# Kernel tuning notes

Hardware: AMD Instinct MI355X
Metric: run time of the kernel (lower is better)

Reference implementation:

```python
import math
import jax, jax.numpy as jnp
import numpy as np

N_HEAD = 16
KNN = 4                     # config.knn_num
MEM_FRAC = 8.0              # config.mem_frac
INFLUENCE = 1.0             # config.knn_softmax_influence
RESID_FOUND = 0.5           # from set_resid_frac(resid_frac=0.5) (assumed split)
RESID_CURR = 0.5


def setup_inputs() -> dict:
    key = jax.random.key(0)
    ks = jax.random.split(key, 7)
    B, T, C, H, M = 1, 1024, 1024, N_HEAD, 8192
    d = C // H
    return {
        "x": jax.random.normal(ks[0], (B, T, C), jnp.float32),
        "c_attn_w": jax.random.normal(ks[1], (3 * C, C), jnp.float32) * 0.02,
        "c_attn_b": jax.random.normal(ks[2], (3 * C,), jnp.float32) * 0.01,
        "c_proj_w": jax.random.normal(ks[3], (C, C), jnp.float32) * 0.02,
        "c_proj_b": jax.random.normal(ks[4], (C,), jnp.float32) * 0.01,
        "key_store": jax.random.normal(ks[5], (H, M, d), jnp.float32),
        "value_store": jax.random.normal(ks[6], (H, M, d), jnp.float32),
    }


def _knn_get(att, k, q, v, key_store, value_store):
    # Faithful vectorized version of knn_get (batch must be 1, as in the
    # original whose scatter offsets i*t are only valid for b==1).
    B, H, T, d = k.shape
    scale = 1.0 / math.sqrt(d)
    # last-query attention row over all keys: (B,H,T)
    a = att[:, :, -1, :]
    # mem_frac thresholding (bookkeeping_frac falsy -> skipped)
    a = jnp.where(a < 1.0 / (MEM_FRAC * T), 0.0, a)
    sel = (a != 0.0)[0]                      # (H,T) selected positions
    kh, qh, vh = k[0], q[0], v[0]            # (H,T,d)
    # exact L2 search = faiss.IndexFlatL2: d2 = |k|^2 - 2 k.s + |s|^2
    d2 = (jnp.sum(kh * kh, -1, keepdims=True)
          - 2.0 * jnp.einsum('htd,hmd->htm', kh, key_store)
          + jnp.sum(key_store * key_store, -1)[:, None, :])   # (H,T,M)
    _, idx = jax.lax.top_k(-d2, KNN)         # (H,T,K) nearest neighbors
    idx = jnp.maximum(idx, 0)                # idx[idx<0]=0
    keys_f = jnp.take_along_axis(key_store[:, None, :, :], idx[..., None], axis=2)   # (H,T,K,d)
    vals_f = jnp.take_along_axis(value_store[:, None, :, :], idx[..., None], axis=2)
    # not resid_only: prepend current key/value -> stack size K+1
    keys_all = jnp.concatenate([kh[:, :, None, :], keys_f], axis=2)   # (H,T,S,d)
    vals_all = jnp.concatenate([vh[:, :, None, :], vals_f], axis=2)
    attf = jnp.einsum('htd,htsd->hts', qh, keys_all) * scale
    attf = jnp.where(jnp.isnan(attf), -jnp.inf, attf)
    w = jax.nn.softmax(attf * INFLUENCE, axis=-1)                     # softmax over the stack dim
    vals = jnp.einsum('hts,htsd->htd', w, vals_all)
    vals = vals * RESID_FOUND + vh * RESID_CURR                       # resid mix branch
    v_new = jnp.where(sel[..., None], vals, vh)                       # scatter back
    return v_new[None]                                                # (1,H,T,d)


def reference(x, c_attn_w, c_attn_b, c_proj_w, c_proj_b, key_store, value_store):
    B, T, C = x.shape
    H = key_store.shape[0]
    d = C // H
    qkv = x @ c_attn_w.T + c_attn_b
    q, k, v = jnp.split(qkv, 3, axis=2)
    heads = lambda t: t.reshape(B, T, H, d).transpose(0, 2, 1, 3)
    q, k, v = heads(q), heads(k), heads(v)
    logits = jnp.einsum('bhqd,bhkd->bhqk', q, k) * (1.0 / math.sqrt(d))
    causal = jnp.tril(jnp.ones((T, T), bool))
    logits = jnp.where(causal, logits, -jnp.inf)
    att = jax.nn.softmax(logits, axis=-1)
    # knn_get runs under torch.no_grad in the original
    v_new = jax.lax.stop_gradient(_knn_get(att, k, q, v, key_store, value_store))
    y = jnp.einsum('bhqk,bhkd->bhqd', att, v_new)   # dropout p=0 (eval)
    y = y.transpose(0, 2, 1, 3).reshape(B, T, C)
    return y @ c_proj_w.T + c_proj_b
```

## Files before the change

kernel.cpp:

```cpp
#include <hip/hip_runtime.h>
#include <math.h>

#define NH 16
#define TT 1024
#define CC 1024
#define DD 64
#define MM 8192
#define MQ 4
#define MQS (MM / MQ)

typedef __attribute__((ext_vector_type(8))) short short8;
typedef __attribute__((ext_vector_type(4))) float f32x4;

__device__ __forceinline__ float wredsum(float x) {
#pragma unroll
  for (int o = 32; o; o >>= 1) x += __shfl_xor(x, o);
  return x;
}
__device__ __forceinline__ unsigned int bf16rn(float x) {
  unsigned int u = __float_as_uint(x);
  return (u + 0x7fffu + ((u >> 16) & 1u)) >> 16;
}
__device__ __forceinline__ float bf16f(unsigned int h) {
  return __uint_as_float(h << 16);
}

__device__ __forceinline__ void ins4(float d, int i, float vd[4], int vi[4]) {
  if (d < vd[3] || (d == vd[3] && i < vi[3])) {
    vd[3] = d; vi[3] = i;
#pragma unroll
    for (int s = 3; s > 0; --s) {
      bool sw = (vd[s] < vd[s - 1]) || (vd[s] == vd[s - 1] && vi[s] < vi[s - 1]);
      if (sw) {
        float td = vd[s]; vd[s] = vd[s - 1]; vd[s - 1] = td;
        int ti = vi[s]; vi[s] = vi[s - 1]; vi[s - 1] = ti;
      }
    }
  }
}

__device__ __forceinline__ void stage_rows8_swz(const char* gRow0, size_t gStride, char* lds, int lane) {
  int rr = lane >> 3;
  int c = (lane & 7) ^ rr;
  __builtin_amdgcn_global_load_lds(
      (const __attribute__((address_space(1))) unsigned int*)(gRow0 + (size_t)rr * gStride + (c << 4)),
      (__attribute__((address_space(3))) unsigned int*)lds, 16, 0, 0);
}

__device__ __forceinline__ void conv_chunk(const float* __restrict__ src,
                                           char* __restrict__ hi, char* __restrict__ lo, int gc) {
  const float* p = src + ((size_t)gc << 3);
  float4 f0 = *(const float4*)p;
  float4 f1 = *(const float4*)(p + 4);
  float f[8] = {f0.x, f0.y, f0.z, f0.w, f1.x, f1.y, f1.z, f1.w};
  short8 hv, lv;
#pragma unroll
  for (int e = 0; e < 8; ++e) {
    unsigned hb = bf16rn(f[e]);
    hv[e] = (short)hb;
    lv[e] = (short)bf16rn(f[e] - bf16f(hb));
  }
  size_t off = (size_t)gc << 4;
  *(short8*)(hi + off) = hv;
  *(short8*)(lo + off) = lv;
}

__device__ __forceinline__ void conv_chunk_hi(const float* __restrict__ src,
                                              char* __restrict__ hi, int gc) {
  const float* p = src + ((size_t)gc << 3);
  float4 f0 = *(const float4*)p;
  float4 f1 = *(const float4*)(p + 4);
  float f[8] = {f0.x, f0.y, f0.z, f0.w, f1.x, f1.y, f1.z, f1.w};
  short8 hv;
#pragma unroll
  for (int e = 0; e < 8; ++e) hv[e] = (short)bf16rn(f[e]);
  *(short8*)(hi + ((size_t)gc << 4)) = hv;
}

__global__ void __launch_bounds__(256) convert_all(
    const float* __restrict__ x, char* __restrict__ xhi, char* __restrict__ xlo,
    const float* __restrict__ Wa, char* __restrict__ wahi, char* __restrict__ walo,
    const float* __restrict__ Wp, char* __restrict__ wphi,
    const float* __restrict__ ks, char* __restrict__ khi, char* __restrict__ klo,
    float* __restrict__ kn2)
{
  int b = blockIdx.x, tid = threadIdx.x;
  if (b < 512) { conv_chunk(x, xhi, xlo, b * 256 + tid); return; }
  if (b < 2048) {
    int gc = (b - 512) * 256 + tid;
    if (gc < 262144) conv_chunk(Wa, wahi, walo, gc);
    else conv_chunk_hi(Wa, wahi, gc);
    return;
  }
  if (b < 2560) { conv_chunk_hi(Wp, wphi, (b - 2048) * 256 + tid); return; }
  int gc = (b - 2560) * 256 + tid;
  const float* p = ks + ((size_t)gc << 3);
  float4 f0 = *(const float4*)p;
  float4 f1 = *(const float4*)(p + 4);
  float f[8] = {f0.x, f0.y, f0.z, f0.w, f1.x, f1.y, f1.z, f1.w};
  float s = 0.f;
  short8 hv, lv;
#pragma unroll
  for (int e = 0; e < 8; ++e) {
    s = fmaf(f[e], f[e], s);
    unsigned hb = bf16rn(f[e]);
    hv[e] = (short)hb;
    lv[e] = (short)bf16rn(f[e] - bf16f(hb));
  }
  size_t off = (size_t)gc << 4;
  *(short8*)(khi + off) = hv;
  *(short8*)(klo + off) = lv;
  s += __shfl_xor(s, 1);
  s += __shfl_xor(s, 2);
  s += __shfl_xor(s, 4);
  if ((tid & 7) == 0) kn2[gc >> 3] = -0.5f * s;
}

__global__ void __launch_bounds__(256) gemm_qkv(
    const char* __restrict__ xhi, const char* __restrict__ xlo,
    const char* __restrict__ wahi, const char* __restrict__ walo,
    const float* __restrict__ ba, char* __restrict__ qhi, char* __restrict__ qlo)
{
  int n0 = blockIdx.x * 128, m0 = blockIdx.y * 64;
  bool vsec = (n0 >= 2048);
  int tid = threadIdx.x, lane = tid & 63, w = tid >> 6;
  int wr = w >> 1, wc = w & 1;
  int lr = lane & 15, lc = lane >> 4;
  __shared__ __align__(16) char smem[49152];
  char* sAhi = smem;
  char* sAlo = smem + 8192;
  char* sBhi = smem + 16384;
  char* sBlo = smem + 32768;
  f32x4 acc[2][4];
#pragma unroll
  for (int i = 0; i < 2; ++i)
#pragma unroll
    for (int j = 0; j < 4; ++j) acc[i][j] = (f32x4){0.f, 0.f, 0.f, 0.f};

  for (int kb = 0; kb < 16; ++kb) {
    if (kb) __syncthreads();
#pragma unroll
    for (int c8 = 0; c8 < 2; ++c8) {
      int r8 = w * 16 + c8 * 8;
      stage_rows8_swz(xhi + (size_t)(m0 + r8) * 2048 + (size_t)kb * 128, 2048, sAhi + r8 * 128, lane);
      if (!vsec)
        stage_rows8_swz(xlo + (size_t)(m0 + r8) * 2048 + (size_t)kb * 128, 2048, sAlo + r8 * 128, lane);
    }
#pragma unroll
    for (int c8 = 0; c8 < 4; ++c8) {
      int r8 = w * 32 + c8 * 8;
      stage_rows8_swz(wahi + (size_t)(n0 + r8) * 2048 + (size_t)kb * 128, 2048, sBhi + r8 * 128, lane);
      if (!vsec)
        stage_rows8_swz(walo + (size_t)(n0 + r8) * 2048 + (size_t)kb * 128, 2048, sBlo + r8 * 128, lane);
    }
    __syncthreads();
#pragma unroll
    for (int kh = 0; kh < 2; ++kh) {
      short8 ah[2], al[2], bh[4], bl[4];
#pragma unroll
      for (int mi = 0; mi < 2; ++mi) {
        int ra = wr * 32 + mi * 16 + lr;
        int ca = ((kh * 4 + lc) ^ (ra & 7)) << 4;
        ah[mi] = *(const short8*)(sAhi + ra * 128 + ca);
        if (!vsec) al[mi] = *(const short8*)(sAlo + ra * 128 + ca);
      }
#pragma unroll
      for (int nj = 0; nj < 4; ++nj) {
        int rb = wc * 64 + nj * 16 + lr;
        int cb = ((kh * 4 + lc) ^ (rb & 7)) << 4;
        bh[nj] = *(const short8*)(sBhi + rb * 128 + cb);
        if (!vsec) bl[nj] = *(const short8*)(sBlo + rb * 128 + cb);
      }
      if (!vsec) {
#pragma unroll
        for (int mi = 0; mi < 2; ++mi)
#pragma unroll
          for (int nj = 0; nj < 4; ++nj) {
            acc[mi][nj] = __builtin_amdgcn_mfma_f32_16x16x32_bf16(ah[mi], bh[nj], acc[mi][nj], 0, 0, 0);
            acc[mi][nj] = __builtin_amdgcn_mfma_f32_16x16x32_bf16(al[mi], bh[nj], acc[mi][nj], 0, 0, 0);
            acc[mi][nj] = __builtin_amdgcn_mfma_f32_16x16x32_bf16(ah[mi], bl[nj], acc[mi][nj], 0, 0, 0);
          }
      } else {
#pragma unroll
        for (int mi = 0; mi < 2; ++mi)
#pragma unroll
          for (int nj = 0; nj < 4; ++nj)
            acc[mi][nj] = __builtin_amdgcn_mfma_f32_16x16x32_bf16(ah[mi], bh[nj], acc[mi][nj], 0, 0, 0);
      }
    }
  }

  __syncthreads();
  char* hbuf = smem + w * 9216;
  char* lbuf = hbuf + 4608;
#pragma unroll
  for (int mi = 0; mi < 2; ++mi)
#pragma unroll
    for (int nj = 0; nj < 4; ++nj)
#pragma unroll
      for (int r = 0; r < 4; ++r) {
        int row = mi * 16 + lc * 4 + r;
        int col = nj * 16 + lr;
        float v = acc[mi][nj][r] + ba[n0 + wc * 64 + col];
        unsigned hb = bf16rn(v);
        *(unsigned short*)(hbuf + row * 144 + col * 2) = (unsigned short)hb;
        if (!vsec)
          *(unsigned short*)(lbuf + row * 144 + col * 2) = (unsigned short)bf16rn(v - bf16f(hb));
      }
#pragma unroll
  for (int ps = 0; ps < 4; ++ps) {
    int rr = ps * 8 + (lane >> 3);
    int c = lane & 7;
    size_t gb = ((size_t)(m0 + wr * 32 + rr) * 3072 + n0 + wc * 64) * 2 + (c << 4);
    *(uint4*)(qhi + gb) = *(const uint4*)(hbuf + rr * 144 + c * 16);
    if (!vsec) *(uint4*)(qlo + gb) = *(const uint4*)(lbuf + rr * 144 + c * 16);
  }
}

#define QSLDS 2304
__global__ void __launch_bounds__(512) qk_softmax(
    const char* __restrict__ qhi, const char* __restrict__ qlo,
    char* __restrict__ attB, float* __restrict__ attlast)
{
  int rb = blockIdx.x, h = blockIdx.y;
  int i0 = rb * 32;
  bool full = (rb == 31);
  int tid = threadIdx.x, lane = tid & 63, w = tid >> 6;
  int wr = w >> 2, wcg = w & 3;
  int lr = lane & 15, lc = lane >> 4;
  __shared__ float redm[2][16][4];
  __shared__ float reds[2][16][4];
  __shared__ __align__(16) char tb[8][QSLDS];

  int iq = i0 + wr * 16 + lr;
  short8 ah[2];
  short8 al[2] = {short8{0,0,0,0,0,0,0,0}, short8{0,0,0,0,0,0,0,0}};
  {
    size_t qb = (size_t)iq * 6144 + h * 128;
#pragma unroll
    for (int kh = 0; kh < 2; ++kh)
      ah[kh] = *(const short8*)(qhi + qb + ((kh * 4 + lc) << 4));
    if (full) {
#pragma unroll
      for (int kh = 0; kh < 2; ++kh)
        al[kh] = *(const short8*)(qlo + qb + ((kh * 4 + lc) << 4));
    }
  }

  f32x4 acc[16];
#pragma unroll
  for (int nt = 0; nt < 16; ++nt) acc[nt] = (f32x4){0.f, 0.f, 0.f, 0.f};

  int maxj = i0 + 31;
#pragma unroll
  for (int nt = 0; nt < 16; ++nt) {
    if (wcg * 256 + nt * 16 <= maxj) {
      int jr = wcg * 256 + nt * 16 + lr;
      size_t kb = (size_t)jr * 6144 + 2048 + h * 128;
      short8 bh[2];
#pragma unroll
      for (int kh = 0; kh < 2; ++kh)
        bh[kh] = *(const short8*)(qhi + kb + ((kh * 4 + lc) << 4));
      if (full) {
        short8 bl[2];
#pragma unroll
        for (int kh = 0; kh < 2; ++kh)
          bl[kh] = *(const short8*)(qlo + kb + ((kh * 4 + lc) << 4));
#pragma unroll
        for (int kh = 0; kh < 2; ++kh) {
          acc[nt] = __builtin_amdgcn_mfma_f32_16x16x32_bf16(ah[kh], bh[kh], acc[nt], 0, 0, 0);
          acc[nt] = __builtin_amdgcn_mfma_f32_16x16x32_bf16(al[kh], bh[kh], acc[nt], 0, 0, 0);
          acc[nt] = __builtin_amdgcn_mfma_f32_16x16x32_bf16(ah[kh], bl[kh], acc[nt], 0, 0, 0);
        }
      } else {
#pragma unroll
        for (int kh = 0; kh < 2; ++kh)
          acc[nt] = __builtin_amdgcn_mfma_f32_16x16x32_bf16(ah[kh], bh[kh], acc[nt], 0, 0, 0);
      }
    }
  }

  int iv[4];
  float pmax[4];
#pragma unroll
  for (int r = 0; r < 4; ++r) {
    iv[r] = i0 + wr * 16 + lc * 4 + r;
    pmax[r] = -INFINITY;
  }
#pragma unroll
  for (int nt = 0; nt < 16; ++nt) {
    if (wcg * 256 + nt * 16 <= maxj) {
      int j = wcg * 256 + nt * 16 + lr;
#pragma unroll
      for (int r = 0; r < 4; ++r) {
        float v = (j <= iv[r]) ? acc[nt][r] * 0.125f : -INFINITY;
        acc[nt][r] = v;
        pmax[r] = fmaxf(pmax[r], v);
      }
    }
  }
#pragma unroll
  for (int o = 1; o <= 8; o <<= 1)
#pragma unroll
    for (int r = 0; r < 4; ++r) pmax[r] = fmaxf(pmax[r], __shfl_xor(pmax[r], o));
  if (lr == 0) {
#pragma unroll
    for (int r = 0; r < 4; ++r) redm[wr][lc * 4 + r][wcg] = pmax[r];
  }
  __syncthreads();
  float rowm[4];
#pragma unroll
  for (int r = 0; r < 4; ++r) {
    float* q = redm[wr][lc * 4 + r];
    rowm[r] = fmaxf(fmaxf(q[0], q[1]), fmaxf(q[2], q[3]));
  }

  float psum[4] = {0.f, 0.f, 0.f, 0.f};
#pragma unroll
  for (int nt = 0; nt < 16; ++nt) {
    if (wcg * 256 + nt * 16 <= maxj) {
#pragma unroll
      for (int r = 0; r < 4; ++r) {
        float e = __expf(acc[nt][r] - rowm[r]);
        acc[nt][r] = e;
        psum[r] += e;
      }
    }
  }
#pragma unroll
  for (int o = 1; o <= 8; o <<= 1)
#pragma unroll
    for (int r = 0; r < 4; ++r) psum[r] += __shfl_xor(psum[r], o);
  if (lr == 0) {
#pragma unroll
    for (int r = 0; r < 4; ++r) reds[wr][lc * 4 + r][wcg] = psum[r];
  }
  __syncthreads();
  float inv[4];
#pragma unroll
  for (int r = 0; r < 4; ++r) {
    float* q = reds[wr][lc * 4 + r];
    inv[r] = 1.0f / (q[0] + q[1] + q[2] + q[3]);
  }

  char* mybuf = tb[w];
  int iv0 = i0 + wr * 16;
  int limit128 = (i0 & ~127) + 128;
#pragma unroll
  for (int cc = 0; cc < 4; ++cc) {
    if (wcg * 256 + cc * 64 < limit128) {
#pragma unroll
      for (int q = 0; q < 4; ++q) {
        int nt = cc * 4 + q;
        int col = q * 16 + lr;
#pragma unroll
        for (int r = 0; r < 4; ++r) {
          int row = lc * 4 + r;
          float v = acc[nt][r] * inv[r];
          *(unsigned short*)(mybuf + row * 144 + col * 2) = (unsigned short)bf16rn(v);
          if (iv[r] == 1023) attlast[(h << 10) + wcg * 256 + cc * 64 + col] = v;
        }
      }
#pragma unroll
      for (int half = 0; half < 2; ++half) {
        int rr = (lane >> 3) + half * 8;
        int c = lane & 7;
        int rowg = iv0 + rr;
        uint4 hv = *(const uint4*)(mybuf + rr * 144 + c * 16);
        size_t basep = ((size_t)h << 21) + ((size_t)rowg << 11)
                     + (size_t)(((wcg << 2) + cc) << 7) + (size_t)(c << 4);
        *(uint4*)(attB + basep) = hv;
      }
    }
  }
}

#define BUFB 16384

#define TOPK_STEP(PAR, DO_STAGE)                                              \
  {                                                                           \
    if (DO_STAGE) {                                                           \
      _Pragma("unroll")                                                       \
      for (int i2 = 0; i2 < 4; ++i2) {                                        \
        __builtin_amdgcn_global_load_lds(                                     \
            (const __attribute__((address_space(1))) unsigned int*)stsrc[i2], \
            (__attribute__((address_space(3))) unsigned int*)(stdst[i2] + ((PAR) ^ 16384)), \
            16, 0, 0);                                                        \
        stsrc[i2] += 8192;                                                    \
      }                                                                       \
    }                                                                         \
    f32x4 acc[4];                                                             \
    _Pragma("unroll")                                                         \
    for (int ms = 0; ms < 4; ++ms)                                            \
      acc[ms] = *(const f32x4*)(knp + ms * 64);                               \
    knp += 256;                                                               \
    _Pragma("unroll")                                                         \
    for (int ms = 0; ms < 4; ++ms) {                                          \
      short8 ah0 = *(const short8*)(frg[ms * 2 + 0] + (PAR));                 \
      short8 al0 = *(const short8*)(frg[ms * 2 + 0] + (PAR) + 8192);          \
      short8 ah1 = *(const short8*)(frg[ms * 2 + 1] + (PAR));                 \
      short8 al1 = *(const short8*)(frg[ms * 2 + 1] + (PAR) + 8192);          \
      acc[ms] = __builtin_amdgcn_mfma_f32_16x16x32_bf16(ah0, bhi[0], acc[ms], 0, 0, 0); \
      acc[ms] = __builtin_amdgcn_mfma_f32_16x16x32_bf16(al0, bhi[0], acc[ms], 0, 0, 0); \
      acc[ms] = __builtin_amdgcn_mfma_f32_16x16x32_bf16(ah0, blo[0], acc[ms], 0, 0, 0); \
      acc[ms] = __builtin_amdgcn_mfma_f32_16x16x32_bf16(ah1, bhi[1], acc[ms], 0, 0, 0); \
      acc[ms] = __builtin_amdgcn_mfma_f32_16x16x32_bf16(al1, bhi[1], acc[ms], 0, 0, 0); \
      acc[ms] = __builtin_amdgcn_mfma_f32_16x16x32_bf16(ah1, blo[1], acc[ms], 0, 0, 0); \
    }                                                                         \
    float pk[16];                                                             \
    _Pragma("unroll")                                                         \
    for (int ms = 0; ms < 4; ++ms)                                            \
      _Pragma("unroll")                                                       \
      for (int r = 0; r < 4; ++r) {                                           \
        unsigned u = __float_as_uint(acc[ms][r]);                             \
        pk[ms * 4 + r] = __uint_as_float((u & ~15u) | (unsigned)(ms * 4 + r)); \
      }                                                                       \
    float mx = pk[0];                                                         \
    _Pragma("unroll")                                                         \
    for (int c = 1; c < 16; ++c) mx = fmaxf(mx, pk[c]);                       \
    while (mx > ba[3]) {                                                      \
      unsigned pb = __float_as_uint(mx);                                      \
      int cl = pb & 15;                                                       \
      ba[3] = mx; bi_[3] = mg0 + ((cl & 12) << 2) + (cl & 3);                 \
      _Pragma("unroll")                                                       \
      for (int s = 3; s > 0; --s)                                             \
        if (ba[s] > ba[s - 1]) {                                              \
          float td = ba[s]; ba[s] = ba[s - 1]; ba[s - 1] = td;                \
          int ti = bi_[s]; bi_[s] = bi_[s - 1]; bi_[s - 1] = ti;              \
        }                                                                     \
      _Pragma("unroll")                                                       \
      for (int c2 = 0; c2 < 16; ++c2)                                         \
        if (pk[c2] == mx) pk[c2] = -3.0e38f;                                  \
      mx = pk[0];                                                             \
      _Pragma("unroll")                                                       \
      for (int c2 = 1; c2 < 16; ++c2) mx = fmaxf(mx, pk[c2]);                 \
    }                                                                         \
    mg0 += 64;                                                                \
    __syncthreads();                                                          \
  }

__global__ void __launch_bounds__(256, 4) topk_mfma(
    const char* __restrict__ qhi, const char* __restrict__ qlo,
    const char* __restrict__ khi, const char* __restrict__ klo,
    const float* __restrict__ kn2, float* __restrict__ pd, int* __restrict__ pi)
{
  int bid = blockIdx.x;
  int h = bid & 15, ttile = (bid >> 4) & 15, mq = bid >> 8;
  int tid = threadIdx.x, lane = tid & 63, w = tid >> 6;
  int t0 = ttile * 64 + w * 16;
  __shared__ __align__(16) char smem[2 * BUFB];

  short8 bhi[2], blo[2];
  {
    int t = t0 + (lane & 15);
    size_t rb = (size_t)t * 6144 + 2048 + h * 128;
#pragma unroll
    for (int kh = 0; kh < 2; ++kh) {
      size_t off = rb + ((kh * 4 + (lane >> 4)) << 4);
      bhi[kh] = *(const short8*)(qhi + off);
      blo[kh] = *(const short8*)(qlo + off);
    }
  }

  const char* ghi = khi + ((size_t)h * MM + (size_t)mq * MQS) * 128;
  const char* glo = klo + ((size_t)h * MM + (size_t)mq * MQS) * 128;
  const char* knp = (const char*)(kn2 + (size_t)h * MM + (size_t)mq * MQS + ((lane >> 4) << 2));

  float ba[4] = {-3.0e38f, -3.0e38f, -3.0e38f, -3.0e38f};
  int   bi_[4] = {-1, -1, -1, -1};

  const char* stsrc[4];
  char* stdst[4];
  {
    int rr = lane >> 3;
    size_t laneoff = (size_t)rr * 128 + (((lane & 7) ^ rr) << 4);
#pragma unroll
    for (int i2 = 0; i2 < 4; ++i2) {
      int s = w * 4 + i2;
      stsrc[i2] = ((s < 8) ? (ghi + s * 1024) : (glo + (s - 8) * 1024)) + laneoff;
      stdst[i2] = smem + s * 1024;
    }
  }
  char* frg[8];
#pragma unroll
  for (int ms = 0; ms < 4; ++ms)
#pragma unroll
    for (int kh = 0; kh < 2; ++kh) {
      int mloc = ms * 16 + (lane & 15);
      int c = kh * 4 + (lane >> 4);
      frg[ms * 2 + kh] = smem + mloc * 128 + ((c ^ (mloc & 7)) << 4);
    }

#pragma unroll
  for (int i2 = 0; i2 < 4; ++i2) {
    __builtin_amdgcn_global_load_lds(
        (const __attribute__((address_space(1))) unsigned int*)stsrc[i2],
        (__attribute__((address_space(3))) unsigned int*)stdst[i2], 16, 0, 0);
    stsrc[i2] += 8192;
  }
  __syncthreads();

  int mg0 = mq * MQS + ((lane >> 4) << 2);
  for (int it2 = 0; it2 < 16; ++it2) {
    TOPK_STEP(0, true)
    TOPK_STEP(16384, (it2 < 15))
  }

  float bd[4];
#pragma unroll
  for (int s = 0; s < 4; ++s) bd[s] = ba[s] * -2.0f;
#pragma unroll
  for (int st = 16; st <= 32; st <<= 1) {
    float sd[4]; int si[4];
#pragma unroll
    for (int s = 0; s < 4; ++s) {
      sd[s] = __shfl_xor(bd[s], st);
      si[s] = __shfl_xor(bi_[s], st);
    }
#pragma unroll
    for (int s = 0; s < 4; ++s) ins4(sd[s], si[s], bd, bi_);
  }
  if (lane < 16) {
    size_t o = (((size_t)mq * NH + h) * TT + (t0 + lane)) * 4;
#pragma unroll
    for (int s = 0; s < 4; ++s) { pd[o + s] = bd[s]; pi[o + s] = bi_[s]; }
  }
}

__global__ void __launch_bounds__(1024) knn_attend(
    const char* __restrict__ qhi,
    const float* __restrict__ attlast,
    const float* __restrict__ pd, const int* __restrict__ pi,
    const float* __restrict__ kstore, const float* __restrict__ vstore,
    char* __restrict__ vThi)
{
  __shared__ __align__(16) unsigned short hiT[64][72];
  int tid = threadIdx.x, lane = tid & 63, w = tid >> 6;
  int h = blockIdx.x >> 4, t0 = (blockIdx.x & 15) << 6;

#pragma unroll
  for (int i = 0; i < 4; ++i) {
    int t = t0 + w * 4 + i;
    int g = (h << 10) + t;

    float fd[4]; int fi[4];
    {
      size_t o = ((size_t)(lane & 3) * (NH * TT) + g) * 4;
#pragma unroll
      for (int s = 0; s < 4; ++s) { fd[s] = pd[o + s]; fi[s] = pi[o + s]; }
#pragma unroll
      for (int st = 1; st <= 2; st <<= 1) {
        float sd[4]; int si[4];
#pragma unroll
        for (int s = 0; s < 4; ++s) {
          sd[s] = __shfl_xor(fd[s], st);
          si[s] = __shfl_xor(fi[s], st);
        }
#pragma unroll
        for (int s = 0; s < 4; ++s) ins4(sd[s], si[s], fd, fi);
      }
    }

    size_t rbq = (size_t)t * 6144 + h * 128 + lane * 2;
    float q = bf16f(*(const unsigned short*)(qhi + rbq));
    float k = bf16f(*(const unsigned short*)(qhi + rbq + 2048));
    float v = bf16f(*(const unsigned short*)(qhi + rbq + 4096));
    float al = attlast[g];
    bool sel = al >= (1.0f / 8192.0f);

    float attf[5], vf[5];
    attf[0] = wredsum(q * k) * 0.125f;
    vf[0] = v;
#pragma unroll
    for (int s = 1; s < 5; ++s) {
      int m = fi[s - 1];
      const float* kp = kstore + ((size_t)h * MM + m) * DD;
      const float* vp = vstore + ((size_t)h * MM + m) * DD;
      attf[s] = wredsum(q * kp[lane]) * 0.125f;
      vf[s] = vp[lane];
    }
    float mx = attf[0];
#pragma unroll
    for (int s = 1; s < 5; ++s) mx = fmaxf(mx, attf[s]);
    float wgt[5], sum = 0.f;
#pragma unroll
    for (int s = 0; s < 5; ++s) { wgt[s] = __expf(attf[s] - mx); sum += wgt[s]; }
    float inv = 1.0f / sum;
    float vals = 0.f;
#pragma unroll
    for (int s = 0; s < 5; ++s) vals = fmaf(wgt[s] * inv, vf[s], vals);
    float r = 0.5f * vals + 0.5f * v;
    float vn = sel ? r : v;

    hiT[lane][t - t0] = (unsigned short)bf16rn(vn);
  }
  __syncthreads();

  if (tid < 512) {
    int r = tid >> 3, c = tid & 7;
    uint4 vv = *(const uint4*)&hiT[r][c * 8];
    char* dst = vThi + (size_t)((h << 6) + r) * 2048 + ((size_t)t0 << 1) + (c << 4);
    *(uint4*)dst = vv;
  }
}

__global__ void __launch_bounds__(256) gemm_attv(
    const char* __restrict__ attB, const char* __restrict__ vThi,
    char* __restrict__ Yhi)
{
  int h = blockIdx.y, m0 = blockIdx.x * 64;
  const char* aBase = attB + ((size_t)h << 21);
  int tid = threadIdx.x, lane = tid & 63, w = tid >> 6;
  int wr = w >> 1, wc = w & 1;
  __shared__ __align__(16) char smem[16384];
  char* sAhi = smem;
  char* sBhi = smem + 8192;
  f32x4 acc[2][2];
#pragma unroll
  for (int i = 0; i < 2; ++i)
#pragma unroll
    for (int j = 0; j < 2; ++j) acc[i][j] = (f32x4){0.f, 0.f, 0.f, 0.f};
  int lr = lane & 15, lc = lane >> 4;
  int kbEnd = (m0 >> 6) + 1;
  for (int kb = 0; kb < kbEnd; ++kb) {
    if (kb) __syncthreads();
#pragma unroll
    for (int c8 = 0; c8 < 2; ++c8) {
      int r8 = w * 16 + c8 * 8;
      stage_rows8_swz(aBase + (size_t)(m0 + r8) * 2048 + (size_t)kb * 128, 2048, sAhi + r8 * 128, lane);
      stage_rows8_swz(vThi + (size_t)((h << 6) + r8) * 2048 + (size_t)kb * 128, 2048, sBhi + r8 * 128, lane);
    }
    __syncthreads();
#pragma unroll
    for (int kh = 0; kh < 2; ++kh) {
      short8 ah[2], bh[2];
#pragma unroll
      for (int f = 0; f < 2; ++f) {
        int ra = wr * 32 + f * 16 + lr;
        int ca = ((kh * 4 + lc) ^ (ra & 7)) << 4;
        ah[f] = *(const short8*)(sAhi + ra * 128 + ca);
        int rbr = wc * 32 + f * 16 + lr;
        int cb = ((kh * 4 + lc) ^ (rbr & 7)) << 4;
        bh[f] = *(const short8*)(sBhi + rbr * 128 + cb);
      }
#pragma unroll
      for (int mi = 0; mi < 2; ++mi)
#pragma unroll
        for (int nj = 0; nj < 2; ++nj)
          acc[mi][nj] = __builtin_amdgcn_mfma_f32_16x16x32_bf16(ah[mi], bh[nj], acc[mi][nj], 0, 0, 0);
    }
  }
#pragma unroll
  for (int mi = 0; mi < 2; ++mi)
#pragma unroll
    for (int nj = 0; nj < 2; ++nj)
#pragma unroll
      for (int r = 0; r < 4; ++r) {
        int m = m0 + wr * 32 + mi * 16 + lc * 4 + r;
        int n = (h << 6) + wc * 32 + nj * 16 + lr;
        size_t off = ((size_t)m * 1024 + n) * 2;
        *(unsigned short*)(Yhi + off) = (unsigned short)bf16rn(acc[mi][nj][r]);
      }
}

__global__ void __launch_bounds__(256) gemm_out(
    const char* __restrict__ yhi,
    const char* __restrict__ wphi,
    const float* __restrict__ bp, float* __restrict__ out)
{
  int n0 = blockIdx.x * 64, m0 = blockIdx.y * 64;
  int tid = threadIdx.x, lane = tid & 63, w = tid >> 6;
  int wr = w >> 1, wc = w & 1;
  int lr = lane & 15, lc = lane >> 4;
  __shared__ __align__(16) char smem[16384];
  char* sAhi = smem;
  char* sBhi = smem + 8192;
  f32x4 acc[2][2];
#pragma unroll
  for (int i = 0; i < 2; ++i)
#pragma unroll
    for (int j = 0; j < 2; ++j) acc[i][j] = (f32x4){0.f, 0.f, 0.f, 0.f};

  for (int kb = 0; kb < 16; ++kb) {
    if (kb) __syncthreads();
#pragma unroll
    for (int c8 = 0; c8 < 2; ++c8) {
      int r8 = w * 16 + c8 * 8;
      stage_rows8_swz(yhi + (size_t)(m0 + r8) * 2048 + (size_t)kb * 128, 2048, sAhi + r8 * 128, lane);
      stage_rows8_swz(wphi + (size_t)(n0 + r8) * 2048 + (size_t)kb * 128, 2048, sBhi + r8 * 128, lane);
    }
    __syncthreads();
#pragma unroll
    for (int kh = 0; kh < 2; ++kh) {
      short8 ah[2], bh[2];
#pragma unroll
      for (int mi = 0; mi < 2; ++mi) {
        int ra = wr * 32 + mi * 16 + lr;
        int ca = ((kh * 4 + lc) ^ (ra & 7)) << 4;
        ah[mi] = *(const short8*)(sAhi + ra * 128 + ca);
      }
#pragma unroll
      for (int nj = 0; nj < 2; ++nj) {
        int rb = wc * 32 + nj * 16 + lr;
        int cb = ((kh * 4 + lc) ^ (rb & 7)) << 4;
        bh[nj] = *(const short8*)(sBhi + rb * 128 + cb);
      }
#pragma unroll
      for (int mi = 0; mi < 2; ++mi)
#pragma unroll
        for (int nj = 0; nj < 2; ++nj)
          acc[mi][nj] = __builtin_amdgcn_mfma_f32_16x16x32_bf16(ah[mi], bh[nj], acc[mi][nj], 0, 0, 0);
    }
  }
#pragma unroll
  for (int mi = 0; mi < 2; ++mi)
#pragma unroll
    for (int nj = 0; nj < 2; ++nj)
#pragma unroll
      for (int r = 0; r < 4; ++r) {
        int m = m0 + wr * 32 + mi * 16 + lc * 4 + r;
        int n = n0 + wc * 32 + nj * 16 + lr;
        out[(size_t)m * 1024 + n] = acc[mi][nj][r] + bp[n];
      }
}

extern "C" void kernel_launch(void* const* d_in, const int* in_sizes, int n_in,
                              void* d_out, int out_size, void* d_ws, size_t ws_size,
                              hipStream_t stream) {
  (void)in_sizes; (void)n_in; (void)out_size; (void)ws_size;
  const float* x  = (const float*)d_in[0];
  const float* Wa = (const float*)d_in[1];
  const float* ba = (const float*)d_in[2];
  const float* Wp = (const float*)d_in[3];
  const float* bp = (const float*)d_in[4];
  const float* Ks = (const float*)d_in[5];
  const float* Vs = (const float*)d_in[6];
  float* out = (float*)d_out;

  char* base = (char*)d_ws;
  char* xhi  = base;
  char* xlo  = base + 0x200000;
  char* wahi = base + 0x400000;
  char* walo = base + 0xA00000;
  char* khi  = base + 0x1000000;
  char* klo  = base + 0x2000000;
  char*  attB = base;
  char* tail = base + 0x4000000;
  char* qhi = tail;
  char* qlo = tail + 0x600000;
  float* attlast = (float*)(tail + 0xC00000);
  float* kn2     = (float*)(tail + 0xC10000);
  float* pd      = (float*)(tail + 0xC90000);
  int*   pi      = (int*)(tail + 0xE90000);
  char* vThi = tail + 0x1090000;
  char* yhi  = tail + 0x1290000;
  char* wphi = tail + 0x1490000;

  hipLaunchKernelGGL(convert_all, dim3(6656), dim3(256), 0, stream,
                     x, xhi, xlo, Wa, wahi, walo, Wp, wphi, Ks, khi, klo, kn2);
  hipLaunchKernelGGL(gemm_qkv, dim3(24, 16), dim3(256), 0, stream,
                     (const char*)xhi, (const char*)xlo, (const char*)wahi, (const char*)walo,
                     ba, qhi, qlo);
  hipLaunchKernelGGL(topk_mfma, dim3(16 * 16 * MQ), dim3(256), 0, stream,
                     (const char*)qhi, (const char*)qlo, (const char*)khi, (const char*)klo,
                     kn2, pd, pi);
  hipLaunchKernelGGL(qk_softmax, dim3(32, 16), dim3(512), 0, stream,
                     (const char*)qhi, (const char*)qlo, attB, attlast);
  hipLaunchKernelGGL(knn_attend, dim3(256), dim3(1024), 0, stream,
                     (const char*)qhi, attlast, pd, pi, Ks, Vs, vThi);
  hipLaunchKernelGGL(gemm_attv, dim3(16, 16), dim3(256), 0, stream,
                     (const char*)attB, (const char*)vThi, yhi);
  hipLaunchKernelGGL(gemm_out, dim3(16, 16), dim3(256), 0, stream,
                     (const char*)yhi, (const char*)wphi, bp, out);
}
```

Measured before the change: 195.3 us.

## Fuse top-k search and QK softmax into one heterogeneous launch

Merges the independent topk_mfma and qk_softmax kernels into a single 1024-block launch. Even blocks run two top-k units side by side (256 threads each, each with its own 32KB LDS half), and odd blocks run one softmax row-block. The aim is to overlap the memory-bound top-k scan with the softmax work and drop one launch. The key store buffers are moved so they no longer alias attB, which is now written concurrently. In exchange, every block reserves 64KB of shared memory and uses 512 threads, which may lower occupancy for the top-k work.

```diff
diff --git a/kernel.cpp b/kernel.cpp
--- a/kernel.cpp
+++ b/kernel.cpp
@@ -217,165 +217,8 @@
   }
 }
 
+#define BUFB 16384
 #define QSLDS 2304
-__global__ void __launch_bounds__(512) qk_softmax(
-    const char* __restrict__ qhi, const char* __restrict__ qlo,
-    char* __restrict__ attB, float* __restrict__ attlast)
-{
-  int rb = blockIdx.x, h = blockIdx.y;
-  int i0 = rb * 32;
-  bool full = (rb == 31);
-  int tid = threadIdx.x, lane = tid & 63, w = tid >> 6;
-  int wr = w >> 2, wcg = w & 3;
-  int lr = lane & 15, lc = lane >> 4;
-  __shared__ float redm[2][16][4];
-  __shared__ float reds[2][16][4];
-  __shared__ __align__(16) char tb[8][QSLDS];
-
-  int iq = i0 + wr * 16 + lr;
-  short8 ah[2];
-  short8 al[2] = {short8{0,0,0,0,0,0,0,0}, short8{0,0,0,0,0,0,0,0}};
-  {
-    size_t qb = (size_t)iq * 6144 + h * 128;
-#pragma unroll
-    for (int kh = 0; kh < 2; ++kh)
-      ah[kh] = *(const short8*)(qhi + qb + ((kh * 4 + lc) << 4));
-    if (full) {
-#pragma unroll
-      for (int kh = 0; kh < 2; ++kh)
-        al[kh] = *(const short8*)(qlo + qb + ((kh * 4 + lc) << 4));
-    }
-  }
-
-  f32x4 acc[16];
-#pragma unroll
-  for (int nt = 0; nt < 16; ++nt) acc[nt] = (f32x4){0.f, 0.f, 0.f, 0.f};
-
-  int maxj = i0 + 31;
-#pragma unroll
-  for (int nt = 0; nt < 16; ++nt) {
-    if (wcg * 256 + nt * 16 <= maxj) {
-      int jr = wcg * 256 + nt * 16 + lr;
-      size_t kb = (size_t)jr * 6144 + 2048 + h * 128;
-      short8 bh[2];
-#pragma unroll
-      for (int kh = 0; kh < 2; ++kh)
-        bh[kh] = *(const short8*)(qhi + kb + ((kh * 4 + lc) << 4));
-      if (full) {
-        short8 bl[2];
-#pragma unroll
-        for (int kh = 0; kh < 2; ++kh)
-          bl[kh] = *(const short8*)(qlo + kb + ((kh * 4 + lc) << 4));
-#pragma unroll
-        for (int kh = 0; kh < 2; ++kh) {
-          acc[nt] = __builtin_amdgcn_mfma_f32_16x16x32_bf16(ah[kh], bh[kh], acc[nt], 0, 0, 0);
-          acc[nt] = __builtin_amdgcn_mfma_f32_16x16x32_bf16(al[kh], bh[kh], acc[nt], 0, 0, 0);
-          acc[nt] = __builtin_amdgcn_mfma_f32_16x16x32_bf16(ah[kh], bl[kh], acc[nt], 0, 0, 0);
-        }
-      } else {
-#pragma unroll
-        for (int kh = 0; kh < 2; ++kh)
-          acc[nt] = __builtin_amdgcn_mfma_f32_16x16x32_bf16(ah[kh], bh[kh], acc[nt], 0, 0, 0);
-      }
-    }
-  }
-
-  int iv[4];
-  float pmax[4];
-#pragma unroll
-  for (int r = 0; r < 4; ++r) {
-    iv[r] = i0 + wr * 16 + lc * 4 + r;
-    pmax[r] = -INFINITY;
-  }
-#pragma unroll
-  for (int nt = 0; nt < 16; ++nt) {
-    if (wcg * 256 + nt * 16 <= maxj) {
-      int j = wcg * 256 + nt * 16 + lr;
-#pragma unroll
-      for (int r = 0; r < 4; ++r) {
-        float v = (j <= iv[r]) ? acc[nt][r] * 0.125f : -INFINITY;
-        acc[nt][r] = v;
-        pmax[r] = fmaxf(pmax[r], v);
-      }
-    }
-  }
-#pragma unroll
-  for (int o = 1; o <= 8; o <<= 1)
-#pragma unroll
-    for (int r = 0; r < 4; ++r) pmax[r] = fmaxf(pmax[r], __shfl_xor(pmax[r], o));
-  if (lr == 0) {
-#pragma unroll
-    for (int r = 0; r < 4; ++r) redm[wr][lc * 4 + r][wcg] = pmax[r];
-  }
-  __syncthreads();
-  float rowm[4];
-#pragma unroll
-  for (int r = 0; r < 4; ++r) {
-    float* q = redm[wr][lc * 4 + r];
-    rowm[r] = fmaxf(fmaxf(q[0], q[1]), fmaxf(q[2], q[3]));
-  }
-
-  float psum[4] = {0.f, 0.f, 0.f, 0.f};
-#pragma unroll
-  for (int nt = 0; nt < 16; ++nt) {
-    if (wcg * 256 + nt * 16 <= maxj) {
-#pragma unroll
-      for (int r = 0; r < 4; ++r) {
-        float e = __expf(acc[nt][r] - rowm[r]);
-        acc[nt][r] = e;
-        psum[r] += e;
-      }
-    }
-  }
-#pragma unroll
-  for (int o = 1; o <= 8; o <<= 1)
-#pragma unroll
-    for (int r = 0; r < 4; ++r) psum[r] += __shfl_xor(psum[r], o);
-  if (lr == 0) {
-#pragma unroll
-    for (int r = 0; r < 4; ++r) reds[wr][lc * 4 + r][wcg] = psum[r];
-  }
-  __syncthreads();
-  float inv[4];
-#pragma unroll
-  for (int r = 0; r < 4; ++r) {
-    float* q = reds[wr][lc * 4 + r];
-    inv[r] = 1.0f / (q[0] + q[1] + q[2] + q[3]);
-  }
-
-  char* mybuf = tb[w];
-  int iv0 = i0 + wr * 16;
-  int limit128 = (i0 & ~127) + 128;
-#pragma unroll
-  for (int cc = 0; cc < 4; ++cc) {
-    if (wcg * 256 + cc * 64 < limit128) {
-#pragma unroll
-      for (int q = 0; q < 4; ++q) {
-        int nt = cc * 4 + q;
-        int col = q * 16 + lr;
-#pragma unroll
-        for (int r = 0; r < 4; ++r) {
-          int row = lc * 4 + r;
-          float v = acc[nt][r] * inv[r];
-          *(unsigned short*)(mybuf + row * 144 + col * 2) = (unsigned short)bf16rn(v);
-          if (iv[r] == 1023) attlast[(h << 10) + wcg * 256 + cc * 64 + col] = v;
-        }
-      }
-#pragma unroll
-      for (int half = 0; half < 2; ++half) {
-        int rr = (lane >> 3) + half * 8;
-        int c = lane & 7;
-        int rowg = iv0 + rr;
-        uint4 hv = *(const uint4*)(mybuf + rr * 144 + c * 16);
-        size_t basep = ((size_t)h << 21) + ((size_t)rowg << 11)
-                     + (size_t)(((wcg << 2) + cc) << 7) + (size_t)(c << 4);
-        *(uint4*)(attB + basep) = hv;
-      }
-    }
-  }
-}
-
-#define BUFB 16384
 
 #define TOPK_STEP(PAR, DO_STAGE)                                              \
   {                                                                           \
@@ -439,91 +282,252 @@
     __syncthreads();                                                          \
   }
 
-__global__ void __launch_bounds__(256, 4) topk_mfma(
+__global__ void __launch_bounds__(512, 4) fused_topk_qk(
     const char* __restrict__ qhi, const char* __restrict__ qlo,
     const char* __restrict__ khi, const char* __restrict__ klo,
-    const float* __restrict__ kn2, float* __restrict__ pd, int* __restrict__ pi)
+    const float* __restrict__ kn2, float* __restrict__ pd, int* __restrict__ pi,
+    char* __restrict__ attB, float* __restrict__ attlast)
 {
+  __shared__ __align__(16) char smem[65536];
   int bid = blockIdx.x;
-  int h = bid & 15, ttile = (bid >> 4) & 15, mq = bid >> 8;
-  int tid = threadIdx.x, lane = tid & 63, w = tid >> 6;
-  int t0 = ttile * 64 + w * 16;
-  __shared__ __align__(16) char smem[2 * BUFB];
-
-  short8 bhi[2], blo[2];
-  {
-    int t = t0 + (lane & 15);
-    size_t rb = (size_t)t * 6144 + 2048 + h * 128;
-#pragma unroll
-    for (int kh = 0; kh < 2; ++kh) {
-      size_t off = rb + ((kh * 4 + (lane >> 4)) << 4);
-      bhi[kh] = *(const short8*)(qhi + off);
-      blo[kh] = *(const short8*)(qlo + off);
-    }
-  }
-
-  const char* ghi = khi + ((size_t)h * MM + (size_t)mq * MQS) * 128;
-  const char* glo = klo + ((size_t)h * MM + (size_t)mq * MQS) * 128;
-  const char* knp = (const char*)(kn2 + (size_t)h * MM + (size_t)mq * MQS + ((lane >> 4) << 2));
-
-  float ba[4] = {-3.0e38f, -3.0e38f, -3.0e38f, -3.0e38f};
-  int   bi_[4] = {-1, -1, -1, -1};
-
-  const char* stsrc[4];
-  char* stdst[4];
-  {
-    int rr = lane >> 3;
-    size_t laneoff = (size_t)rr * 128 + (((lane & 7) ^ rr) << 4);
+  int tid = threadIdx.x;
+
+  if ((bid & 1) == 0) {
+    int uid = (bid & ~1) + (tid >> 8);
+    char* usmem = smem + ((tid >> 8) << 15);
+    int ltid = tid & 255;
+    int h = uid & 15, ttile = (uid >> 4) & 15, mq = uid >> 8;
+    int lane = ltid & 63, w = ltid >> 6;
+    int t0 = ttile * 64 + w * 16;
+
+    short8 bhi[2], blo[2];
+    {
+      int t = t0 + (lane & 15);
+      size_t rb = (size_t)t * 6144 + 2048 + h * 128;
+#pragma unroll
+      for (int kh = 0; kh < 2; ++kh) {
+        size_t off = rb + ((kh * 4 + (lane >> 4)) << 4);
+        bhi[kh] = *(const short8*)(qhi + off);
+        blo[kh] = *(const short8*)(qlo + off);
+      }
+    }
+
+    const char* ghi = khi + ((size_t)h * MM + (size_t)mq * MQS) * 128;
+    const char* glo = klo + ((size_t)h * MM + (size_t)mq * MQS) * 128;
+    const char* knp = (const char*)(kn2 + (size_t)h * MM + (size_t)mq * MQS + ((lane >> 4) << 2));
+
+    float ba[4] = {-3.0e38f, -3.0e38f, -3.0e38f, -3.0e38f};
+    int   bi_[4] = {-1, -1, -1, -1};
+
+    const char* stsrc[4];
+    char* stdst[4];
+    {
+      int rr = lane >> 3;
+      size_t laneoff = (size_t)rr * 128 + (((lane & 7) ^ rr) << 4);
+#pragma unroll
+      for (int i2 = 0; i2 < 4; ++i2) {
+        int s = w * 4 + i2;
+        stsrc[i2] = ((s < 8) ? (ghi + s * 1024) : (glo + (s - 8) * 1024)) + laneoff;
+        stdst[i2] = usmem + s * 1024;
+      }
+    }
+    char* frg[8];
+#pragma unroll
+    for (int ms = 0; ms < 4; ++ms)
+#pragma unroll
+      for (int kh = 0; kh < 2; ++kh) {
+        int mloc = ms * 16 + (lane & 15);
+        int c = kh * 4 + (lane >> 4);
+        frg[ms * 2 + kh] = usmem + mloc * 128 + ((c ^ (mloc & 7)) << 4);
+      }
+
 #pragma unroll
     for (int i2 = 0; i2 < 4; ++i2) {
-      int s = w * 4 + i2;
-      stsrc[i2] = ((s < 8) ? (ghi + s * 1024) : (glo + (s - 8) * 1024)) + laneoff;
-      stdst[i2] = smem + s * 1024;
-    }
-  }
-  char* frg[8];
-#pragma unroll
-  for (int ms = 0; ms < 4; ++ms)
-#pragma unroll
-    for (int kh = 0; kh < 2; ++kh) {
-      int mloc = ms * 16 + (lane & 15);
-      int c = kh * 4 + (lane >> 4);
-      frg[ms * 2 + kh] = smem + mloc * 128 + ((c ^ (mloc & 7)) << 4);
-    }
-
-#pragma unroll
-  for (int i2 = 0; i2 < 4; ++i2) {
-    __builtin_amdgcn_global_load_lds(
-        (const __attribute__((address_space(1))) unsigned int*)stsrc[i2],
-        (__attribute__((address_space(3))) unsigned int*)stdst[i2], 16, 0, 0);
-    stsrc[i2] += 8192;
-  }
-  __syncthreads();
-
-  int mg0 = mq * MQS + ((lane >> 4) << 2);
-  for (int it2 = 0; it2 < 16; ++it2) {
-    TOPK_STEP(0, true)
-    TOPK_STEP(16384, (it2 < 15))
-  }
-
-  float bd[4];
-#pragma unroll
-  for (int s = 0; s < 4; ++s) bd[s] = ba[s] * -2.0f;
-#pragma unroll
-  for (int st = 16; st <= 32; st <<= 1) {
-    float sd[4]; int si[4];
-#pragma unroll
-    for (int s = 0; s < 4; ++s) {
-      sd[s] = __shfl_xor(bd[s], st);
-      si[s] = __shfl_xor(bi_[s], st);
-    }
-#pragma unroll
-    for (int s = 0; s < 4; ++s) ins4(sd[s], si[s], bd, bi_);
-  }
-  if (lane < 16) {
-    size_t o = (((size_t)mq * NH + h) * TT + (t0 + lane)) * 4;
-#pragma unroll
-    for (int s = 0; s < 4; ++s) { pd[o + s] = bd[s]; pi[o + s] = bi_[s]; }
+      __builtin_amdgcn_global_load_lds(
+          (const __attribute__((address_space(1))) unsigned int*)stsrc[i2],
+          (__attribute__((address_space(3))) unsigned int*)stdst[i2], 16, 0, 0);
+      stsrc[i2] += 8192;
+    }
+    __syncthreads();
+
+    int mg0 = mq * MQS + ((lane >> 4) << 2);
+    for (int it2 = 0; it2 < 16; ++it2) {
+      TOPK_STEP(0, true)
+      TOPK_STEP(16384, (it2 < 15))
+    }
+
+    float bd[4];
+#pragma unroll
+    for (int s = 0; s < 4; ++s) bd[s] = ba[s] * -2.0f;
+#pragma unroll
+    for (int st = 16; st <= 32; st <<= 1) {
+      float sd[4]; int si[4];
+#pragma unroll
+      for (int s = 0; s < 4; ++s) {
+        sd[s] = __shfl_xor(bd[s], st);
+        si[s] = __shfl_xor(bi_[s], st);
+      }
+#pragma unroll
+      for (int s = 0; s < 4; ++s) ins4(sd[s], si[s], bd, bi_);
+    }
+    if (lane < 16) {
+      size_t o = (((size_t)mq * NH + h) * TT + (t0 + lane)) * 4;
+#pragma unroll
+      for (int s = 0; s < 4; ++s) { pd[o + s] = bd[s]; pi[o + s] = bi_[s]; }
+    }
+  } else {
+    int qb = bid >> 1;
+    int rb = qb & 31, h = qb >> 5;
+    int i0 = rb * 32;
+    bool full = (rb == 31);
+    int lane = tid & 63, w = tid >> 6;
+    int wr = w >> 2, wcg = w & 3;
+    int lr = lane & 15, lc = lane >> 4;
+    float (*redm)[16][4] = (float (*)[16][4])smem;
+    float (*reds)[16][4] = (float (*)[16][4])(smem + 512);
+    char* tbb = smem + 1024;
+
+    int iq = i0 + wr * 16 + lr;
+    short8 ah[2];
+    short8 al[2] = {short8{0,0,0,0,0,0,0,0}, short8{0,0,0,0,0,0,0,0}};
+    {
+      size_t qb2 = (size_t)iq * 6144 + h * 128;
+#pragma unroll
+      for (int kh = 0; kh < 2; ++kh)
+        ah[kh] = *(const short8*)(qhi + qb2 + ((kh * 4 + lc) << 4));
+      if (full) {
+#pragma unroll
+        for (int kh = 0; kh < 2; ++kh)
+          al[kh] = *(const short8*)(qlo + qb2 + ((kh * 4 + lc) << 4));
+      }
+    }
+
+    f32x4 acc[16];
+#pragma unroll
+    for (int nt = 0; nt < 16; ++nt) acc[nt] = (f32x4){0.f, 0.f, 0.f, 0.f};
+
+    int maxj = i0 + 31;
+#pragma unroll
+    for (int nt = 0; nt < 16; ++nt) {
+      if (wcg * 256 + nt * 16 <= maxj) {
+        int jr = wcg * 256 + nt * 16 + lr;
+        size_t kb = (size_t)jr * 6144 + 2048 + h * 128;
+        short8 bh[2];
+#pragma unroll
+        for (int kh = 0; kh < 2; ++kh)
+          bh[kh] = *(const short8*)(qhi + kb + ((kh * 4 + lc) << 4));
+        if (full) {
+          short8 bl[2];
+#pragma unroll
+          for (int kh = 0; kh < 2; ++kh)
+            bl[kh] = *(const short8*)(qlo + kb + ((kh * 4 + lc) << 4));
+#pragma unroll
+          for (int kh = 0; kh < 2; ++kh) {
+            acc[nt] = __builtin_amdgcn_mfma_f32_16x16x32_bf16(ah[kh], bh[kh], acc[nt], 0, 0, 0);
+            acc[nt] = __builtin_amdgcn_mfma_f32_16x16x32_bf16(al[kh], bh[kh], acc[nt], 0, 0, 0);
+            acc[nt] = __builtin_amdgcn_mfma_f32_16x16x32_bf16(ah[kh], bl[kh], acc[nt], 0, 0, 0);
+          }
+        } else {
+#pragma unroll
+          for (int kh = 0; kh < 2; ++kh)
+            acc[nt] = __builtin_amdgcn_mfma_f32_16x16x32_bf16(ah[kh], bh[kh], acc[nt], 0, 0, 0);
+        }
+      }
+    }
+
+    int iv[4];
+    float pmax[4];
+#pragma unroll
+    for (int r = 0; r < 4; ++r) {
+      iv[r] = i0 + wr * 16 + lc * 4 + r;
+      pmax[r] = -INFINITY;
+    }
+#pragma unroll
+    for (int nt = 0; nt < 16; ++nt) {
+      if (wcg * 256 + nt * 16 <= maxj) {
+        int j = wcg * 256 + nt * 16 + lr;
+#pragma unroll
+        for (int r = 0; r < 4; ++r) {
+          float v = (j <= iv[r]) ? acc[nt][r] * 0.125f : -INFINITY;
+          acc[nt][r] = v;
+          pmax[r] = fmaxf(pmax[r], v);
+        }
+      }
+    }
+#pragma unroll
+    for (int o = 1; o <= 8; o <<= 1)
+#pragma unroll
+      for (int r = 0; r < 4; ++r) pmax[r] = fmaxf(pmax[r], __shfl_xor(pmax[r], o));
+    if (lr == 0) {
+#pragma unroll
+      for (int r = 0; r < 4; ++r) redm[wr][lc * 4 + r][wcg] = pmax[r];
+    }
+    __syncthreads();
+    float rowm[4];
+#pragma unroll
+    for (int r = 0; r < 4; ++r) {
+      float* q = redm[wr][lc * 4 + r];
+      rowm[r] = fmaxf(fmaxf(q[0], q[1]), fmaxf(q[2], q[3]));
+    }
+
+    float psum[4] = {0.f, 0.f, 0.f, 0.f};
+#pragma unroll
+    for (int nt = 0; nt < 16; ++nt) {
+      if (wcg * 256 + nt * 16 <= maxj) {
+#pragma unroll
+        for (int r = 0; r < 4; ++r) {
+          float e = __expf(acc[nt][r] - rowm[r]);
+          acc[nt][r] = e;
+          psum[r] += e;
+        }
+      }
+    }
+#pragma unroll
+    for (int o = 1; o <= 8; o <<= 1)
+#pragma unroll
+      for (int r = 0; r < 4; ++r) psum[r] += __shfl_xor(psum[r], o);
+    if (lr == 0) {
+#pragma unroll
+      for (int r = 0; r < 4; ++r) reds[wr][lc * 4 + r][wcg] = psum[r];
+    }
+    __syncthreads();
+    float inv[4];
+#pragma unroll
+    for (int r = 0; r < 4; ++r) {
+      float* q = reds[wr][lc * 4 + r];
+      inv[r] = 1.0f / (q[0] + q[1] + q[2] + q[3]);
+    }
+
+    char* mybuf = tbb + w * QSLDS;
+    int iv0 = i0 + wr * 16;
+    int limit128 = (i0 & ~127) + 128;
+#pragma unroll
+    for (int cc = 0; cc < 4; ++cc) {
+      if (wcg * 256 + cc * 64 < limit128) {
+#pragma unroll
+        for (int q = 0; q < 4; ++q) {
+          int nt = cc * 4 + q;
+          int col = q * 16 + lr;
+#pragma unroll
+          for (int r = 0; r < 4; ++r) {
+            int row = lc * 4 + r;
+            float v = acc[nt][r] * inv[r];
+            *(unsigned short*)(mybuf + row * 144 + col * 2) = (unsigned short)bf16rn(v);
+            if (iv[r] == 1023) attlast[(h << 10) + wcg * 256 + cc * 64 + col] = v;
+          }
+        }
+#pragma unroll
+        for (int half = 0; half < 2; ++half) {
+          int rr = (lane >> 3) + half * 8;
+          int c = lane & 7;
+          int rowg = iv0 + rr;
+          uint4 hv = *(const uint4*)(mybuf + rr * 144 + c * 16);
+          size_t basep = ((size_t)h << 21) + ((size_t)rowg << 11)
+                       + (size_t)(((wcg << 2) + cc) << 7) + (size_t)(c << 4);
+          *(uint4*)(attB + basep) = hv;
+        }
+      }
+    }
   }
 }
 
@@ -742,9 +746,9 @@
   char* xlo  = base + 0x200000;
   char* wahi = base + 0x400000;
   char* walo = base + 0xA00000;
-  char* khi  = base + 0x1000000;
-  char* klo  = base + 0x2000000;
   char*  attB = base;
+  char* khi  = base + 0x2000000;
+  char* klo  = base + 0x3000000;
   char* tail = base + 0x4000000;
   char* qhi = tail;
   char* qlo = tail + 0x600000;
@@ -761,11 +765,9 @@
   hipLaunchKernelGGL(gemm_qkv, dim3(24, 16), dim3(256), 0, stream,
                      (const char*)xhi, (const char*)xlo, (const char*)wahi, (const char*)walo,
                      ba, qhi, qlo);
-  hipLaunchKernelGGL(topk_mfma, dim3(16 * 16 * MQ), dim3(256), 0, stream,
+  hipLaunchKernelGGL(fused_topk_qk, dim3(1024), dim3(512), 0, stream,
                      (const char*)qhi, (const char*)qlo, (const char*)khi, (const char*)klo,
-                     kn2, pd, pi);
-  hipLaunchKernelGGL(qk_softmax, dim3(32, 16), dim3(512), 0, stream,
-                     (const char*)qhi, (const char*)qlo, attB, attlast);
+                     kn2, pd, pi, attB, attlast);
   hipLaunchKernelGGL(knn_attend, dim3(256), dim3(1024), 0, stream,
                      (const char*)qhi, attlast, pd, pi, Ks, Vs, vThi);
   hipLaunchKernelGGL(gemm_attv, dim3(16, 16), dim3(256), 0, stream,
```

Measured after the change: 223.1 us. 1.14x slower.
